# Kernel tuning notes

Hardware: AMD Instinct MI355X
Metric: run time of the kernel (lower is better)

## Reference

```python
import jax, jax.numpy as jnp
import numpy as np

NUM_HEADS = 16
HEAD_DIM = 64  # dim_qkv // num_heads


def setup_inputs() -> dict:
    key = jax.random.key(0)
    ks = jax.random.split(key, 6)
    B, N, D = 2, 2048, 1024
    s = 1.0 / np.sqrt(D)
    x = jax.random.normal(ks[0], (B, N, D), dtype=jnp.float32)
    Wq = jax.random.normal(ks[1], (D, D), dtype=jnp.float32) * s
    Wk = jax.random.normal(ks[2], (D, D), dtype=jnp.float32) * s
    Wv = jax.random.normal(ks[3], (D, D), dtype=jnp.float32) * s
    Wo = jax.random.normal(ks[4], (D, D), dtype=jnp.float32) * s
    z = jnp.zeros((D,), dtype=jnp.float32)
    return {"x": x, "Wq": Wq, "bq": z, "Wk": Wk, "bk": z,
            "Wv": Wv, "bv": z, "Wo": Wo, "bo": z}


def _split_heads(t):
    # [B, N, H*dh] -> [B, H, N, dh]
    B, N, _ = t.shape
    return t.reshape(B, N, NUM_HEADS, HEAD_DIM).transpose(0, 2, 1, 3)


def reference(x, Wq, bq, Wk, bk, Wv, bv, Wo, bo):
    q = _split_heads(x @ Wq + bq)
    k = _split_heads(x @ Wk + bk)
    v = _split_heads(x @ Wv + bv)
    scores = jnp.einsum('bhnd,bhmd->bhnm', q, k) / jnp.sqrt(
        jnp.asarray(HEAD_DIM, dtype=x.dtype))
    attn = jax.nn.softmax(scores, axis=-1)
    heads = jnp.einsum('bhnm,bhmd->bhnd', attn, v)  # [B, H, N, dh]
    B, H, N, dh = heads.shape
    merged = heads.transpose(0, 2, 1, 3).reshape(B, N, H * dh)
    # dropout is identity in deterministic/eval mode
    return merged @ Wo + bo
```

## Files before the change

kernel.cpp:

```cpp
#include <hip/hip_runtime.h>
#include <hip/hip_bf16.h>

typedef __bf16 bf16;
typedef __attribute__((ext_vector_type(8))) __bf16 bf16x8;
typedef __attribute__((ext_vector_type(4))) __bf16 bf16x4;
typedef __attribute__((ext_vector_type(4))) float f32x4;
typedef __attribute__((ext_vector_type(16))) float f32x16;
typedef unsigned int uint;

#define MFMA16(a, b, c) __builtin_amdgcn_mfma_f32_16x16x32_bf16(a, b, c, 0, 0, 0)
#define MFMA32(a, b, c) __builtin_amdgcn_mfma_f32_32x32x16_bf16(a, b, c, 0, 0, 0)

#define GLOAD_LDS(gp, lp) \
  __builtin_amdgcn_global_load_lds( \
      (const __attribute__((address_space(1))) void*)(gp), \
      (__attribute__((address_space(3))) void*)(lp), 16, 0, 0)

#define QSCALE 0.18033688011112042f

__device__ __forceinline__ uint pack2(float a, float b) {
  unsigned short x = __builtin_bit_cast(unsigned short, (bf16)a);
  unsigned short y = __builtin_bit_cast(unsigned short, (bf16)b);
  return (uint)x | ((uint)y << 16);
}

__global__ __launch_bounds__(256) void prep_kernel(
    const float* __restrict__ x, bf16* __restrict__ y,
    const float* __restrict__ W0, const float* __restrict__ W1,
    const float* __restrict__ W2, const float* __restrict__ W3,
    bf16* __restrict__ T0, bf16* __restrict__ T1,
    bf16* __restrict__ T2, bf16* __restrict__ T3) {
  const int bid = blockIdx.x;
  if (bid < 2048) {
    int i = (bid * 256 + threadIdx.x) * 8;
    float4 a = *(const float4*)(x + i);
    float4 b = *(const float4*)(x + i + 4);
    bf16x8 v;
    v[0] = (bf16)a.x; v[1] = (bf16)a.y; v[2] = (bf16)a.z; v[3] = (bf16)a.w;
    v[4] = (bf16)b.x; v[5] = (bf16)b.y; v[6] = (bf16)b.z; v[7] = (bf16)b.w;
    *(bf16x8*)(y + i) = v;
    return;
  }
  const int wq = bid - 2048;
  const int z = wq >> 10, rem = wq & 1023;
  const float* W; bf16* T;
  switch (z) {
    case 0: W = W0; T = T0; break;
    case 1: W = W1; T = T1; break;
    case 2: W = W2; T = T2; break;
    default: W = W3; T = T3; break;
  }
  const float scl = (z == 0) ? QSCALE : 1.0f;
  __shared__ float tile[32][33];
  int tx = threadIdx.x & 31;
  int ty = threadIdx.x >> 5;
  int bx = (rem & 31) * 32, by = (rem >> 5) * 32;
#pragma unroll
  for (int i = 0; i < 32; i += 8)
    tile[ty + i][tx] = W[(size_t)(by + ty + i) * 1024 + bx + tx];
  __syncthreads();
#pragma unroll
  for (int i = 0; i < 32; i += 8)
    T[(size_t)(bx + ty + i) * 1024 + by + tx] = (bf16)(tile[tx][ty + i] * scl);
}

__global__ __launch_bounds__(256, 2) void gemm_qkv_kernel(
    const bf16* __restrict__ A, const bf16* __restrict__ Bt,
    const float* __restrict__ b0, const float* __restrict__ b1,
    const float* __restrict__ b2, bf16* __restrict__ o0,
    bf16* __restrict__ o1, bf16* __restrict__ o2) {
  __shared__ bf16 As[128 * 64];
  __shared__ bf16 Bs[128 * 64];
  const int f = blockIdx.y * 24 + blockIdx.x;
  const int wg = (f % 8) * 96 + f / 8;
  const int bn = wg % 24, bm = wg / 24;
  const int t = threadIdx.x;
  const int lane = t & 63, wid = t >> 6;
  const int wy = wid >> 1, wx = wid & 1;
  const int lr = lane & 15, lg = lane >> 4;
  const bf16* Arow = A + (size_t)bm * 128 * 1024;
  const bf16* Brow = Bt + (size_t)bn * 128 * 1024;
  f32x4 acc[4][4] = {};

  for (int k0 = 0; k0 < 1024; k0 += 64) {
    __syncthreads();
#pragma unroll
    for (int i = 0; i < 4; i++) {
      int off = i * 256 + t;
      int row = off >> 3, ch = off & 7;
      int gch = ch ^ (row & 7);
      GLOAD_LDS(Arow + (size_t)row * 1024 + k0 + gch * 8, As + off * 8);
    }
#pragma unroll
    for (int i = 0; i < 4; i++) {
      int off = i * 256 + t;
      int row = off >> 3, ch = off & 7;
      int gch = ch ^ (row & 7);
      GLOAD_LDS(Brow + (size_t)row * 1024 + k0 + gch * 8, Bs + off * 8);
    }
    __syncthreads();
#pragma unroll
    for (int kh = 0; kh < 2; kh++) {
      bf16x8 af[4], bfr[4];
#pragma unroll
      for (int i = 0; i < 4; i++) {
        int row = wy * 64 + i * 16 + lr;
        int c = kh * 4 + lg;
        af[i] = *(const bf16x8*)(As + row * 64 + ((c ^ (row & 7)) << 3));
      }
#pragma unroll
      for (int j = 0; j < 4; j++) {
        int row = wx * 64 + j * 16 + lr;
        int c = kh * 4 + lg;
        bfr[j] = *(const bf16x8*)(Bs + row * 64 + ((c ^ (row & 7)) << 3));
      }
#pragma unroll
      for (int i = 0; i < 4; i++)
#pragma unroll
        for (int j = 0; j < 4; j++)
          acc[i][j] = MFMA16(af[i], bfr[j], acc[i][j]);
    }
  }

  const int seg = bn >> 3;
  const float* bias = (seg == 0) ? b0 : (seg == 1 ? b1 : b2);
  const float bscale = (seg == 0) ? QSCALE : 1.0f;

#pragma unroll
  for (int i = 0; i < 4; i++) {
    const int rowb = bm * 128 + wy * 64 + i * 16 + lg * 4;
#pragma unroll
    for (int j = 0; j < 4; j++) {
      const int np = bn * 128 + wx * 64 + j * 16 + lr;
      const int col = np & 1023;
      const float bv = bias[col] * bscale;
      const int h = col >> 6, d = col & 63;
      const int bb = rowb >> 11, nn = rowb & 2047;
      if (seg == 2) {
        bf16x4 pk;
#pragma unroll
        for (int r = 0; r < 4; r++) pk[r] = (bf16)(acc[i][j][r] + bv);
        *(bf16x4*)(o2 + (((size_t)bb * 16 + h) * 64 + d) * 2048 + nn) = pk;
      } else {
        bf16* dst = (seg == 0) ? o0 : o1;
#pragma unroll
        for (int r = 0; r < 4; r++)
          dst[(((size_t)bb * 16 + h) * 2048 + nn + r) * 64 + d] =
              (bf16)(acc[i][j][r] + bv);
      }
    }
  }
}

__global__ __launch_bounds__(256, 2) void gemmo_kernel(
    const bf16* __restrict__ A, const bf16* __restrict__ Bt,
    const float* __restrict__ bias, float* __restrict__ out) {
  __shared__ bf16 As[128 * 64];
  __shared__ bf16 Bs[64 * 64];
  const int f = blockIdx.y * 16 + blockIdx.x;
  const int wg = (f & 7) * 64 + (f >> 3);
  const int bn = wg & 15, bm = wg >> 4;
  const int t = threadIdx.x;
  const int lane = t & 63, wid = t >> 6;
  const int wy = wid >> 1, wx = wid & 1;
  const int lr = lane & 15, lg = lane >> 4;
  const bf16* Arow = A + (size_t)bm * 128 * 1024;
  const bf16* Brow = Bt + (size_t)bn * 64 * 1024;
  f32x4 acc[4][2] = {};

  for (int k0 = 0; k0 < 1024; k0 += 64) {
    __syncthreads();
#pragma unroll
    for (int i = 0; i < 4; i++) {
      int off = i * 256 + t;
      int row = off >> 3, ch = off & 7;
      int gch = ch ^ (row & 7);
      GLOAD_LDS(Arow + (size_t)row * 1024 + k0 + gch * 8, As + off * 8);
    }
#pragma unroll
    for (int i = 0; i < 2; i++) {
      int off = i * 256 + t;
      int row = off >> 3, ch = off & 7;
      int gch = ch ^ (row & 7);
      GLOAD_LDS(Brow + (size_t)row * 1024 + k0 + gch * 8, Bs + off * 8);
    }
    __syncthreads();
#pragma unroll
    for (int kh = 0; kh < 2; kh++) {
      bf16x8 af[4], bfr[2];
#pragma unroll
      for (int i = 0; i < 4; i++) {
        int row = wy * 64 + i * 16 + lr;
        int c = kh * 4 + lg;
        af[i] = *(const bf16x8*)(As + row * 64 + ((c ^ (row & 7)) << 3));
      }
#pragma unroll
      for (int j = 0; j < 2; j++) {
        int row = wx * 32 + j * 16 + lr;
        int c = kh * 4 + lg;
        bfr[j] = *(const bf16x8*)(Bs + row * 64 + ((c ^ (row & 7)) << 3));
      }
#pragma unroll
      for (int i = 0; i < 4; i++)
#pragma unroll
        for (int j = 0; j < 2; j++)
          acc[i][j] = MFMA16(af[i], bfr[j], acc[i][j]);
    }
  }

#pragma unroll
  for (int i = 0; i < 4; i++) {
    const int rowb = bm * 128 + wy * 64 + i * 16 + lg * 4;
#pragma unroll
    for (int j = 0; j < 2; j++) {
      const int col = bn * 64 + wx * 32 + j * 16 + lr;
      const float bv = bias[col];
#pragma unroll
      for (int r = 0; r < 4; r++)
        out[(size_t)(rowb + r) * 1024 + col] = acc[i][j][r] + bv;
    }
  }
}

__global__ __launch_bounds__(512, 4) void attn_kernel(
    const bf16* __restrict__ Q, const bf16* __restrict__ K,
    const bf16* __restrict__ Vt, bf16* __restrict__ Mg) {
  __shared__ bf16 Kl[2][2][4096];
  __shared__ bf16 Vl[2][2][4096];
  const int t = threadIdx.x;
  const int lane = t & 63, w = t >> 6;
  const int half = w >> 2, wq = w & 3;
  const int l31 = lane & 31, hi = lane >> 5;
  const int f = blockIdx.y * 16 + blockIdx.x;
  const int xcd = f & 7, slot = f >> 3;
  const int bh = xcd * 4 + (slot >> 4);
  const int bx = slot & 15;
  const int b = bh >> 4, h = bh & 15;
  const bf16* Qh = Q + (size_t)bh * 2048 * 64;
  const bf16* KhH = K + (size_t)bh * 2048 * 64 + (size_t)half * 1024 * 64;
  const bf16* VhH = Vt + (size_t)bh * 64 * 2048 + half * 1024;
  const int q_row = bx * 128 + wq * 32 + l31;

  bf16x8 qf[4];
#pragma unroll
  for (int dblk = 0; dblk < 4; dblk++)
    qf[dblk] = *(const bf16x8*)(Qh + (size_t)q_row * 64 + dblk * 16 + hi * 8);

  bf16x8 onesA;
  {
    bf16 ov = (l31 == 0) ? (bf16)1.0f : (bf16)0.0f;
#pragma unroll
    for (int e = 0; e < 8; e++) onesA[e] = ov;
  }

  f32x16 o0 = {}, o1 = {}, osum = {};
  const int th = t & 255;

#define STAGE(kt_, buf_)                                                      \
  {                                                                           \
    _Pragma("unroll") for (int i = 0; i < 2; i++) {                           \
      int off = i * 256 + th;                                                 \
      int row = off >> 3, ch = off & 7;                                       \
      int gch = ch ^ (row & 7);                                               \
      GLOAD_LDS(KhH + (size_t)(kt_) * 4096 + row * 64 + gch * 8,              \
                &Kl[half][buf_][off * 8]);                                    \
      GLOAD_LDS(VhH + (size_t)row * 2048 + (kt_) * 64 + gch * 8,              \
                &Vl[half][buf_][off * 8]);                                    \
    }                                                                         \
  }

  STAGE(0, 0);
  __syncthreads();

  for (int kt = 0; kt < 16; kt++) {
    const int cur = kt & 1;
    if (kt < 15) STAGE(kt + 1, cur ^ 1);

    f32x16 s0 = {}, s1 = {};
    __builtin_amdgcn_s_setprio(1);
#pragma unroll
    for (int dblk = 0; dblk < 4; dblk++) {
      const int c = dblk * 2 + hi;
      const int r0 = l31, r1 = 32 + l31;
      bf16x8 kf0 = *(const bf16x8*)&Kl[half][cur][r0 * 64 + ((c ^ (r0 & 7)) << 3)];
      bf16x8 kf1 = *(const bf16x8*)&Kl[half][cur][r1 * 64 + ((c ^ (r1 & 7)) << 3)];
      s0 = MFMA32(kf0, qf[dblk], s0);
      s1 = MFMA32(kf1, qf[dblk], s1);
    }
    __builtin_amdgcn_s_setprio(0);

#pragma unroll
    for (int r = 0; r < 16; r++) {
      s0[r] = __builtin_amdgcn_exp2f(s0[r]);
      s1[r] = __builtin_amdgcn_exp2f(s1[r]);
    }

    uint prc[8], prd[8];
#pragma unroll
    for (int si = 0; si < 4; si++) {
      prc[si] = pack2(s0[4 * si + 0], s0[4 * si + 1]);
      prd[si] = pack2(s0[4 * si + 2], s0[4 * si + 3]);
      prc[4 + si] = pack2(s1[4 * si + 0], s1[4 * si + 1]);
      prd[4 + si] = pack2(s1[4 * si + 2], s1[4 * si + 3]);
    }

    __builtin_amdgcn_s_setprio(1);
#pragma unroll
    for (int kbl = 0; kbl < 4; kbl++) {
      const int sb = (kbl >> 1) * 4 + (kbl & 1) * 2;
      auto rc = __builtin_amdgcn_permlane32_swap(prc[sb], prc[sb + 1], false, false);
      auto rd = __builtin_amdgcn_permlane32_swap(prd[sb], prd[sb + 1], false, false);
      union { uint u[4]; bf16x8 v; } pf;
      pf.u[0] = rc[0];
      pf.u[1] = rd[0];
      pf.u[2] = rc[1];
      pf.u[3] = rd[1];

      const int c = kbl * 2 + hi;
      const int r0 = l31, r1 = 32 + l31;
      bf16x8 vt0 = *(const bf16x8*)&Vl[half][cur][r0 * 64 + ((c ^ (r0 & 7)) << 3)];
      bf16x8 vt1 = *(const bf16x8*)&Vl[half][cur][r1 * 64 + ((c ^ (r1 & 7)) << 3)];
      o0 = MFMA32(vt0, pf.v, o0);
      o1 = MFMA32(vt1, pf.v, o1);
      osum = MFMA32(onesA, pf.v, osum);
    }
    __builtin_amdgcn_s_setprio(0);

    __syncthreads();
  }

  uint lu = __builtin_bit_cast(uint, osum[0]);
  auto lb = __builtin_amdgcn_permlane32_swap(lu, lu, false, false);
  const float den = __builtin_bit_cast(float, (uint)lb[0]);

  float* ma = (float*)&Kl[0][0][0];
  float* mb = (float*)&Vl[0][0][0];
  const int mi = (wq * 64 + lane) * 17;
  if (half == 1) {
#pragma unroll
    for (int si = 0; si < 16; si++) {
      ma[mi + si] = o0[si];
      mb[mi + si] = o1[si];
    }
    ma[mi + 16] = den;
  }
  __syncthreads();
  if (half == 0) {
    const float inv = 1.f / (den + ma[mi + 16]);
    bf16* orow = Mg + ((size_t)b * 2048 + q_row) * 1024 + h * 64;
#pragma unroll
    for (int si = 0; si < 4; si++) {
      bf16x4 p0, p1;
#pragma unroll
      for (int r = 0; r < 4; r++) {
        p0[r] = (bf16)((o0[4 * si + r] + ma[mi + 4 * si + r]) * inv);
        p1[r] = (bf16)((o1[4 * si + r] + mb[mi + 4 * si + r]) * inv);
      }
      *(bf16x4*)(orow + si * 8 + hi * 4) = p0;
      *(bf16x4*)(orow + 32 + si * 8 + hi * 4) = p1;
    }
  }
}

extern "C" void kernel_launch(void* const* d_in, const int* in_sizes, int n_in,
                              void* d_out, int out_size, void* d_ws, size_t ws_size,
                              hipStream_t stream) {
  const float* x  = (const float*)d_in[0];
  const float* Wq = (const float*)d_in[1];
  const float* bq = (const float*)d_in[2];
  const float* Wk = (const float*)d_in[3];
  const float* bk = (const float*)d_in[4];
  const float* Wv = (const float*)d_in[5];
  const float* bv = (const float*)d_in[6];
  const float* Wo = (const float*)d_in[7];
  const float* bo = (const float*)d_in[8];
  float* out = (float*)d_out;
  char* ws = (char*)d_ws;
  const size_t MiB = 1u << 20;

  bf16* Xb   = (bf16*)(ws);
  bf16* Mg   = Xb;
  bf16* Wqkv = (bf16*)(ws + 8 * MiB);
  bf16* WoT  = (bf16*)(ws + 14 * MiB);
  bf16* Qb   = (bf16*)(ws + 16 * MiB);
  bf16* Kb   = (bf16*)(ws + 24 * MiB);
  bf16* Vtb  = (bf16*)(ws + 32 * MiB);

  prep_kernel<<<6144, 256, 0, stream>>>(
      x, Xb, Wq, Wk, Wv, Wo, Wqkv, Wqkv + (1u << 20), Wqkv + (2u << 20), WoT);
  gemm_qkv_kernel<<<dim3(24, 32), 256, 0, stream>>>(
      Xb, Wqkv, bq, bk, bv, Qb, Kb, Vtb);
  attn_kernel<<<dim3(16, 32), 512, 0, stream>>>(Qb, Kb, Vtb, Mg);
  gemmo_kernel<<<dim3(16, 32), 256, 0, stream>>>(Mg, WoT, bo, out);
  (void)in_sizes; (void)n_in; (void)out_size; (void)ws_size;
}
```

Before: 110.2 us.

## Load K/V fragments directly from global memory into registers, dropping LDS staging

The attention kernel no longer stages K and V tiles into double-buffered shared memory through global_load_lds. Each wave now reads its K and V MFMA fragments straight from global memory into registers. This removes the per-iteration __syncthreads and most of the LDS footprint, keeping only small float buffers for merging the two halves. The cost is that the four waves in each half each fetch the same K/V data, relying on cache hits, and the strided V loads give up the swizzled LDS reuse. The denominator read is also changed so that lanes in the lower half use their own osum value instead of the permuted one.

```diff
diff --git a/kernel.cpp b/kernel.cpp
--- a/kernel.cpp
+++ b/kernel.cpp
@@ -225,8 +225,8 @@
 __global__ __launch_bounds__(512, 4) void attn_kernel(
     const bf16* __restrict__ Q, const bf16* __restrict__ K,
     const bf16* __restrict__ Vt, bf16* __restrict__ Mg) {
-  __shared__ bf16 Kl[2][2][4096];
-  __shared__ bf16 Vl[2][2][4096];
+  __shared__ float ma[4 * 64 * 17];
+  __shared__ float mb[4 * 64 * 17];
   const int t = threadIdx.x;
   const int lane = t & 63, w = t >> 6;
   const int half = w >> 2, wq = w & 3;
@@ -253,39 +253,30 @@
     for (int e = 0; e < 8; e++) onesA[e] = ov;
   }
 
+  const bf16* kp0 = KhH + l31 * 64 + hi * 8;
+  const bf16* kp1 = kp0 + 32 * 64;
+  const bf16* vp0 = VhH + (size_t)l31 * 2048 + hi * 8;
+  const bf16* vp1 = VhH + (size_t)(32 + l31) * 2048 + hi * 8;
+
   f32x16 o0 = {}, o1 = {}, osum = {};
-  const int th = t & 255;
-
-#define STAGE(kt_, buf_)                                                      \
-  {                                                                           \
-    _Pragma("unroll") for (int i = 0; i < 2; i++) {                           \
-      int off = i * 256 + th;                                                 \
-      int row = off >> 3, ch = off & 7;                                       \
-      int gch = ch ^ (row & 7);                                               \
-      GLOAD_LDS(KhH + (size_t)(kt_) * 4096 + row * 64 + gch * 8,              \
-                &Kl[half][buf_][off * 8]);                                    \
-      GLOAD_LDS(VhH + (size_t)row * 2048 + (kt_) * 64 + gch * 8,              \
-                &Vl[half][buf_][off * 8]);                                    \
-    }                                                                         \
-  }
-
-  STAGE(0, 0);
-  __syncthreads();
 
   for (int kt = 0; kt < 16; kt++) {
-    const int cur = kt & 1;
-    if (kt < 15) STAGE(kt + 1, cur ^ 1);
+    const int ko = kt * 4096;
+    const int vo = kt * 64;
+
+    bf16x8 kf0[4], kf1[4];
+#pragma unroll
+    for (int dblk = 0; dblk < 4; dblk++) {
+      kf0[dblk] = *(const bf16x8*)(kp0 + ko + dblk * 16);
+      kf1[dblk] = *(const bf16x8*)(kp1 + ko + dblk * 16);
+    }
 
     f32x16 s0 = {}, s1 = {};
     __builtin_amdgcn_s_setprio(1);
 #pragma unroll
     for (int dblk = 0; dblk < 4; dblk++) {
-      const int c = dblk * 2 + hi;
-      const int r0 = l31, r1 = 32 + l31;
-      bf16x8 kf0 = *(const bf16x8*)&Kl[half][cur][r0 * 64 + ((c ^ (r0 & 7)) << 3)];
-      bf16x8 kf1 = *(const bf16x8*)&Kl[half][cur][r1 * 64 + ((c ^ (r1 & 7)) << 3)];
-      s0 = MFMA32(kf0, qf[dblk], s0);
-      s1 = MFMA32(kf1, qf[dblk], s1);
+      s0 = MFMA32(kf0[dblk], qf[dblk], s0);
+      s1 = MFMA32(kf1[dblk], qf[dblk], s1);
     }
     __builtin_amdgcn_s_setprio(0);
 
@@ -304,37 +295,39 @@
       prd[4 + si] = pack2(s1[4 * si + 2], s1[4 * si + 3]);
     }
 
-    __builtin_amdgcn_s_setprio(1);
-#pragma unroll
-    for (int kbl = 0; kbl < 4; kbl++) {
-      const int sb = (kbl >> 1) * 4 + (kbl & 1) * 2;
-      auto rc = __builtin_amdgcn_permlane32_swap(prc[sb], prc[sb + 1], false, false);
-      auto rd = __builtin_amdgcn_permlane32_swap(prd[sb], prd[sb + 1], false, false);
-      union { uint u[4]; bf16x8 v; } pf;
-      pf.u[0] = rc[0];
-      pf.u[1] = rd[0];
-      pf.u[2] = rc[1];
-      pf.u[3] = rd[1];
-
-      const int c = kbl * 2 + hi;
-      const int r0 = l31, r1 = 32 + l31;
-      bf16x8 vt0 = *(const bf16x8*)&Vl[half][cur][r0 * 64 + ((c ^ (r0 & 7)) << 3)];
-      bf16x8 vt1 = *(const bf16x8*)&Vl[half][cur][r1 * 64 + ((c ^ (r1 & 7)) << 3)];
-      o0 = MFMA32(vt0, pf.v, o0);
-      o1 = MFMA32(vt1, pf.v, o1);
-      osum = MFMA32(onesA, pf.v, osum);
-    }
-    __builtin_amdgcn_s_setprio(0);
-
-    __syncthreads();
+#pragma unroll
+    for (int kp = 0; kp < 2; kp++) {
+      bf16x8 va[2], vb[2];
+#pragma unroll
+      for (int j = 0; j < 2; j++) {
+        const int c16 = (kp * 2 + j) * 16;
+        va[j] = *(const bf16x8*)(vp0 + vo + c16);
+        vb[j] = *(const bf16x8*)(vp1 + vo + c16);
+      }
+      __builtin_amdgcn_s_setprio(1);
+#pragma unroll
+      for (int j = 0; j < 2; j++) {
+        const int kbl = kp * 2 + j;
+        const int sb = (kbl >> 1) * 4 + (kbl & 1) * 2;
+        auto rc = __builtin_amdgcn_permlane32_swap(prc[sb], prc[sb + 1], false, false);
+        auto rd = __builtin_amdgcn_permlane32_swap(prd[sb], prd[sb + 1], false, false);
+        union { uint u[4]; bf16x8 v; } pf;
+        pf.u[0] = rc[0];
+        pf.u[1] = rd[0];
+        pf.u[2] = rc[1];
+        pf.u[3] = rd[1];
+        o0 = MFMA32(va[j], pf.v, o0);
+        o1 = MFMA32(vb[j], pf.v, o1);
+        osum = MFMA32(onesA, pf.v, osum);
+      }
+      __builtin_amdgcn_s_setprio(0);
+    }
   }
 
   uint lu = __builtin_bit_cast(uint, osum[0]);
   auto lb = __builtin_amdgcn_permlane32_swap(lu, lu, false, false);
-  const float den = __builtin_bit_cast(float, (uint)lb[0]);
-
-  float* ma = (float*)&Kl[0][0][0];
-  float* mb = (float*)&Vl[0][0][0];
+  const float den = hi ? __builtin_bit_cast(float, (uint)lb[0]) : osum[0];
+
   const int mi = (wq * 64 + lane) * 17;
   if (half == 1) {
 #pragma unroll
```

After: 204.3 us. 1.85x slower.

## Rewrite QKV GEMM as 256x256 tile, 8-wave, double-buffered ping-pong pipeline

Applied to the files above, without the earlier changes.

Replaces the 128x128, 4-wave QKV projection GEMM with a 256x256-tile kernel using 8 waves and double-buffered LDS. Global-to-LDS loads for tile k+2 are issued while MFMAs run on the current tile, and register fragment banks are split into quadrants so LDS reads interleave with MFMA groups under explicit barriers and waitcnt. The aim is to hide load latency and raise arithmetic intensity per block. The cost is a grid of only 192 blocks, which may underfill the GPU, plus much higher LDS and register use.

```diff
diff --git a/kernel.cpp b/kernel.cpp
--- a/kernel.cpp
+++ b/kernel.cpp
@@ -64,92 +64,123 @@
     T[(size_t)(bx + ty + i) * 1024 + by + tx] = (bf16)(tile[tx][ty + i] * scl);
 }
 
-__global__ __launch_bounds__(256, 2) void gemm_qkv_kernel(
+__global__ __launch_bounds__(512, 2) void gemm_qkv8_kernel(
     const bf16* __restrict__ A, const bf16* __restrict__ Bt,
     const float* __restrict__ b0, const float* __restrict__ b1,
     const float* __restrict__ b2, bf16* __restrict__ o0,
     bf16* __restrict__ o1, bf16* __restrict__ o2) {
-  __shared__ bf16 As[128 * 64];
-  __shared__ bf16 Bs[128 * 64];
-  const int f = blockIdx.y * 24 + blockIdx.x;
-  const int wg = (f % 8) * 96 + f / 8;
-  const int bn = wg % 24, bm = wg / 24;
+  __shared__ bf16 As[2][16384];
+  __shared__ bf16 Bs[2][16384];
   const int t = threadIdx.x;
   const int lane = t & 63, wid = t >> 6;
-  const int wy = wid >> 1, wx = wid & 1;
+  const int wm = wid >> 2, wn = wid & 3;
   const int lr = lane & 15, lg = lane >> 4;
-  const bf16* Arow = A + (size_t)bm * 128 * 1024;
-  const bf16* Brow = Bt + (size_t)bn * 128 * 1024;
-  f32x4 acc[4][4] = {};
-
-  for (int k0 = 0; k0 < 1024; k0 += 64) {
-    __syncthreads();
-#pragma unroll
-    for (int i = 0; i < 4; i++) {
-      int off = i * 256 + t;
-      int row = off >> 3, ch = off & 7;
-      int gch = ch ^ (row & 7);
-      GLOAD_LDS(Arow + (size_t)row * 1024 + k0 + gch * 8, As + off * 8);
-    }
-#pragma unroll
-    for (int i = 0; i < 4; i++) {
-      int off = i * 256 + t;
-      int row = off >> 3, ch = off & 7;
-      int gch = ch ^ (row & 7);
-      GLOAD_LDS(Brow + (size_t)row * 1024 + k0 + gch * 8, Bs + off * 8);
-    }
-    __syncthreads();
-#pragma unroll
-    for (int kh = 0; kh < 2; kh++) {
-      bf16x8 af[4], bfr[4];
-#pragma unroll
-      for (int i = 0; i < 4; i++) {
-        int row = wy * 64 + i * 16 + lr;
-        int c = kh * 4 + lg;
-        af[i] = *(const bf16x8*)(As + row * 64 + ((c ^ (row & 7)) << 3));
-      }
-#pragma unroll
-      for (int j = 0; j < 4; j++) {
-        int row = wx * 64 + j * 16 + lr;
-        int c = kh * 4 + lg;
-        bfr[j] = *(const bf16x8*)(Bs + row * 64 + ((c ^ (row & 7)) << 3));
-      }
-#pragma unroll
-      for (int i = 0; i < 4; i++)
-#pragma unroll
-        for (int j = 0; j < 4; j++)
-          acc[i][j] = MFMA16(af[i], bfr[j], acc[i][j]);
-    }
-  }
-
-  const int seg = bn >> 3;
+  const int f = blockIdx.x;
+  const int wg = (f & 7) * 24 + (f >> 3);
+  const int bn = wg % 12, bm = wg / 12;
+  const bf16* Ag = A + (size_t)bm * 256 * 1024;
+  const bf16* Bg = Bt + (size_t)bn * 256 * 1024;
+
+  f32x4 acc[8][4] = {};
+  bf16x8 ra0[2][4], ra1[2][4], rb0[2][2], rb1[2][2];
+
+#define GSTAGE_A(kt2, bb)                                                 \
+  { _Pragma("unroll") for (int ii = 0; ii < 4; ii++) {                    \
+      int off = ii * 512 + t;                                             \
+      int row = off >> 3, ch = off & 7;                                   \
+      int gch = ch ^ (row & 7);                                           \
+      GLOAD_LDS(Ag + (size_t)row * 1024 + (kt2) * 64 + gch * 8,           \
+                &As[bb][off * 8]); } }
+#define GSTAGE_B(kt2, bb)                                                 \
+  { _Pragma("unroll") for (int ii = 0; ii < 4; ii++) {                    \
+      int off = ii * 512 + t;                                             \
+      int row = off >> 3, ch = off & 7;                                   \
+      int gch = ch ^ (row & 7);                                           \
+      GLOAD_LDS(Bg + (size_t)row * 1024 + (kt2) * 64 + gch * 8,           \
+                &Bs[bb][off * 8]); } }
+#define GLOAD_ABANK(bank, mq, bb)                                         \
+  { _Pragma("unroll") for (int kh = 0; kh < 2; kh++)                      \
+    _Pragma("unroll") for (int ii = 0; ii < 4; ii++) {                    \
+      int row = wm * 128 + (mq) * 64 + ii * 16 + lr;                      \
+      int c = kh * 4 + lg;                                                \
+      bank[kh][ii] =                                                      \
+          *(const bf16x8*)&As[bb][row * 64 + ((c ^ (row & 7)) << 3)]; } }
+#define GLOAD_BBANK(bank, nq, bb)                                         \
+  { _Pragma("unroll") for (int kh = 0; kh < 2; kh++)                      \
+    _Pragma("unroll") for (int jj = 0; jj < 2; jj++) {                    \
+      int row = wn * 64 + (nq) * 32 + jj * 16 + lr;                       \
+      int c = kh * 4 + lg;                                                \
+      bank[kh][jj] =                                                      \
+          *(const bf16x8*)&Bs[bb][row * 64 + ((c ^ (row & 7)) << 3)]; } }
+#define GQUAD(mq, nq, ab, bb2)                                            \
+  { __builtin_amdgcn_s_setprio(1);                                        \
+    _Pragma("unroll") for (int kh = 0; kh < 2; kh++)                      \
+    _Pragma("unroll") for (int ii = 0; ii < 4; ii++)                      \
+    _Pragma("unroll") for (int jj = 0; jj < 2; jj++)                      \
+      acc[(mq) * 4 + ii][(nq) * 2 + jj] = MFMA16(                         \
+          ab[kh][ii], bb2[kh][jj], acc[(mq) * 4 + ii][(nq) * 2 + jj]);    \
+    __builtin_amdgcn_s_setprio(0); }
+#define GBAR() asm volatile("s_barrier" ::: "memory")
+
+  GSTAGE_A(0, 0); GSTAGE_B(0, 0);
+  GSTAGE_A(1, 1); GSTAGE_B(1, 1);
+  asm volatile("s_waitcnt vmcnt(8)" ::: "memory");
+  GBAR();
+  GLOAD_ABANK(ra0, 0, 0);
+  GLOAD_BBANK(rb0, 0, 0);
+
+  for (int kt = 0; kt < 16; kt++) {
+    const int cur = kt & 1, nxt = cur ^ 1;
+    GLOAD_ABANK(ra1, 1, cur);
+    GQUAD(0, 0, ra0, rb0);
+    GBAR();
+    GLOAD_BBANK(rb1, 1, cur);
+    GQUAD(1, 0, ra1, rb0);
+    asm volatile("s_waitcnt vmcnt(0)" ::: "memory");
+    GBAR();
+    if (kt < 15) GLOAD_BBANK(rb0, 0, nxt);
+    if (kt < 14) GSTAGE_A(kt + 2, cur);
+    GQUAD(1, 1, ra1, rb1);
+    GBAR();
+    if (kt < 14) GSTAGE_B(kt + 2, cur);
+    GQUAD(0, 1, ra0, rb1);
+    if (kt < 15) GLOAD_ABANK(ra0, 0, nxt);
+    GBAR();
+  }
+
+  const int seg = bn >> 2;
   const float* bias = (seg == 0) ? b0 : (seg == 1 ? b1 : b2);
   const float bscale = (seg == 0) ? QSCALE : 1.0f;
 
 #pragma unroll
-  for (int i = 0; i < 4; i++) {
-    const int rowb = bm * 128 + wy * 64 + i * 16 + lg * 4;
-#pragma unroll
-    for (int j = 0; j < 4; j++) {
-      const int np = bn * 128 + wx * 64 + j * 16 + lr;
-      const int col = np & 1023;
-      const float bv = bias[col] * bscale;
-      const int h = col >> 6, d = col & 63;
-      const int bb = rowb >> 11, nn = rowb & 2047;
-      if (seg == 2) {
-        bf16x4 pk;
-#pragma unroll
-        for (int r = 0; r < 4; r++) pk[r] = (bf16)(acc[i][j][r] + bv);
-        *(bf16x4*)(o2 + (((size_t)bb * 16 + h) * 64 + d) * 2048 + nn) = pk;
-      } else {
-        bf16* dst = (seg == 0) ? o0 : o1;
-#pragma unroll
-        for (int r = 0; r < 4; r++)
-          dst[(((size_t)bb * 16 + h) * 2048 + nn + r) * 64 + d] =
-              (bf16)(acc[i][j][r] + bv);
-      }
-    }
-  }
+  for (int mq = 0; mq < 2; mq++)
+#pragma unroll
+    for (int i = 0; i < 4; i++) {
+      const int rowb = bm * 256 + wm * 128 + mq * 64 + i * 16 + lg * 4;
+      const int bb_ = rowb >> 11, nn = rowb & 2047;
+#pragma unroll
+      for (int nq = 0; nq < 2; nq++)
+#pragma unroll
+        for (int j = 0; j < 2; j++) {
+          const f32x4 av = acc[mq * 4 + i][nq * 2 + j];
+          const int np = bn * 256 + wn * 64 + nq * 32 + j * 16 + lr;
+          const int col = np & 1023;
+          const float bv = bias[col] * bscale;
+          const int h = col >> 6, d = col & 63;
+          if (seg == 2) {
+            bf16x4 pk;
+#pragma unroll
+            for (int r = 0; r < 4; r++) pk[r] = (bf16)(av[r] + bv);
+            *(bf16x4*)(o2 + (((size_t)bb_ * 16 + h) * 64 + d) * 2048 + nn) = pk;
+          } else {
+            bf16* dst = (seg == 0) ? o0 : o1;
+#pragma unroll
+            for (int r = 0; r < 4; r++)
+              dst[(((size_t)bb_ * 16 + h) * 2048 + nn + r) * 64 + d] =
+                  (bf16)(av[r] + bv);
+          }
+        }
+    }
 }
 
 __global__ __launch_bounds__(256, 2) void gemmo_kernel(
@@ -256,7 +287,7 @@
   f32x16 o0 = {}, o1 = {}, osum = {};
   const int th = t & 255;
 
-#define STAGE(kt_, buf_)                                                      \
+#define STAGE_KV(kt_, buf_)                                                   \
   {                                                                           \
     _Pragma("unroll") for (int i = 0; i < 2; i++) {                           \
       int off = i * 256 + th;                                                 \
@@ -269,12 +300,12 @@
     }                                                                         \
   }
 
-  STAGE(0, 0);
+  STAGE_KV(0, 0);
   __syncthreads();
 
   for (int kt = 0; kt < 16; kt++) {
     const int cur = kt & 1;
-    if (kt < 15) STAGE(kt + 1, cur ^ 1);
+    if (kt < 15) STAGE_KV(kt + 1, cur ^ 1);
 
     f32x16 s0 = {}, s1 = {};
     __builtin_amdgcn_s_setprio(1);
@@ -388,7 +419,7 @@
 
   prep_kernel<<<6144, 256, 0, stream>>>(
       x, Xb, Wq, Wk, Wv, Wo, Wqkv, Wqkv + (1u << 20), Wqkv + (2u << 20), WoT);
-  gemm_qkv_kernel<<<dim3(24, 32), 256, 0, stream>>>(
+  gemm_qkv8_kernel<<<192, 512, 0, stream>>>(
       Xb, Wqkv, bq, bk, bv, Qb, Kb, Vtb);
   attn_kernel<<<dim3(16, 32), 512, 0, stream>>>(Qb, Kb, Vtb, Mg);
   gemmo_kernel<<<dim3(16, 32), 256, 0, stream>>>(Mg, WoT, bo, out);
```

Result: slower. 115.3 us (+4.6%).
